# Kernel optimization log

Hardware: AMD Instinct MI355X
Metric: run time of the kernel (lower is better)

## Reference

```python
import jax, jax.numpy as jnp
import numpy as np

H = 450       # hidden_size (JTNN decoder default)
V = 800       # junction-tree vocab size
N_NODES = 4000
N_MESS = 6000
K = 6         # max neighbors (padded)
B = 256       # number of trees / roots
DH = 450      # netD hidden size
DEPTH = 15


def setup_inputs() -> dict:
    key = jax.random.key(0)
    ks = jax.random.split(key, 16)

    def w(k, shape, fan_in):
        return jax.random.normal(k, shape, dtype=jnp.float32) / np.float32(np.sqrt(fan_in))

    inp = {}
    inp["fnode"] = jax.random.randint(ks[0], (N_NODES,), 0, V)
    inp["fmess"] = jax.random.randint(ks[1], (N_MESS,), 0, N_NODES)
    inp["node_graph"] = jax.random.randint(ks[2], (N_NODES, K), 0, N_MESS)
    inp["mess_graph"] = jax.random.randint(ks[3], (N_MESS, K), 0, N_MESS)
    inp["root_idx"] = jax.random.randint(ks[4], (B,), 0, N_NODES)
    # Generator (JTNN decoder GRU) params; weights stored torch-style [out, in]
    inp["emb"] = w(ks[5], (V, H), H)
    inp["W_z_w"] = w(ks[6], (H, 2 * H), 2 * H)
    inp["W_z_b"] = jnp.zeros((H,), jnp.float32)
    inp["W_r_w"] = w(ks[7], (H, H), H)          # bias=False in JTNN
    inp["U_r_w"] = w(ks[8], (H, H), H)
    inp["U_r_b"] = jnp.zeros((H,), jnp.float32)
    inp["W_h_w"] = w(ks[9], (H, 2 * H), 2 * H)
    inp["W_h_b"] = jnp.zeros((H,), jnp.float32)
    # netD: Linear(2H,DH) -> LeakyReLU(0.1) -> Linear(DH,DH) -> LeakyReLU(0.1) -> Linear(DH,1)
    inp["D1_w"] = w(ks[10], (DH, 2 * H), 2 * H)
    inp["D1_b"] = jnp.zeros((DH,), jnp.float32)
    inp["D2_w"] = w(ks[11], (DH, DH), DH)
    inp["D2_b"] = jnp.zeros((DH,), jnp.float32)
    inp["D3_w"] = w(ks[12], (1, DH), DH)
    inp["D3_b"] = jnp.zeros((1,), jnp.float32)
    inp["depth"] = DEPTH
    return inp


def _generator(fnode, fmess, node_graph, mess_graph, root_idx,
               emb, W_z_w, W_z_b, W_r_w, U_r_w, U_r_b, W_h_w, W_h_b, depth):
    fnode_e = emb[fnode]                      # [N, H] embedding lookup
    x = fnode_e[fmess]                        # [M, H] source-node features per message
    M = fmess.shape[0]
    mask = jnp.ones((M, 1), jnp.float32).at[0].set(0.0)   # message 0 is padding
    h0 = jnp.zeros((M, emb.shape[1]), jnp.float32)

    def step(h, _):
        h_nei = h[mess_graph]                 # [M, K, H] gather of incoming messages
        sum_h = h_nei.sum(axis=1)             # [M, H]
        z = jax.nn.sigmoid(jnp.concatenate([x, sum_h], axis=-1) @ W_z_w.T + W_z_b)
        r = jax.nn.sigmoid((x @ W_r_w.T)[:, None, :] + h_nei @ U_r_w.T + U_r_b)
        sum_gh = (r * h_nei).sum(axis=1)
        pre_h = jnp.tanh(jnp.concatenate([x, sum_gh], axis=-1) @ W_h_w.T + W_h_b)
        h_new = ((1.0 - z) * sum_h + z * pre_h) * mask
        return h_new, None

    h, _ = jax.lax.scan(step, h0, None, length=depth)
    mess_nei = h[node_graph].sum(axis=1)      # [N, H]
    node_vecs = jnp.concatenate([fnode_e, mess_nei], axis=-1)   # [N, 2H]
    return node_vecs[root_idx]                # [B, 2H]


def reference(fnode, fmess, node_graph, mess_graph, root_idx,
              emb, W_z_w, W_z_b, W_r_w, U_r_w, U_r_b, W_h_w, W_h_b,
              D1_w, D1_b, D2_w, D2_b, D3_w, D3_b, depth):
    root_vecs = _generator(fnode, fmess, node_graph, mess_graph, root_idx,
                           emb, W_z_w, W_z_b, W_r_w, U_r_w, U_r_b, W_h_w, W_h_b, depth)
    h1 = jax.nn.leaky_relu(root_vecs @ D1_w.T + D1_b, 0.1)
    h2 = jax.nn.leaky_relu(h1 @ D2_w.T + D2_b, 0.1)
    score = (h2 @ D3_w.T + D3_b).squeeze(-1)  # [B] discriminator scores
    return score
```

## Files before the change

### kernel.cpp

```cpp
#include <hip/hip_runtime.h>
#include <stdint.h>
#include <stddef.h>

#define NMSG   6000
#define NNODE  4000
#define HDIM   450
#define KNEI   6
#define NB     256
#define KP     480
#define MP     6016
#define NPAD   512
#define DEPTH_C 15
#define GX     96
#define GROWS  6016

typedef unsigned short u16;
typedef __attribute__((ext_vector_type(8))) short short8;
typedef __attribute__((ext_vector_type(4))) float f32x4;

__device__ __forceinline__ float b2f(u16 h) { return __uint_as_float(((unsigned)h) << 16); }
__device__ __forceinline__ u16 f2b(float f) {
    unsigned u = __float_as_uint(f);
    return (u16)((u + 0x7FFFu + ((u >> 16) & 1u)) >> 16);
}
__device__ __forceinline__ void fsplit(float f, u16& hi, u16& lo) {
    u16 h = f2b(f);
    hi = h;
    lo = f2b(f - b2f(h));
}
__device__ __forceinline__ float gload(const void* p, size_t i, int isb) {
    return isb ? b2f(((const u16*)p)[i]) : ((const float*)p)[i];
}

__device__ __forceinline__ void gload_lds16(const void* g, void* l) {
    __builtin_amdgcn_global_load_lds((const __attribute__((address_space(1))) unsigned int*)g,
                                     (__attribute__((address_space(3))) unsigned int*)l,
                                     16, 0, 0);
}

__device__ __forceinline__ int xcd_row(int b) {
    if (b >= 5632) return b;
    int c = b & 7, u = b >> 3;
    return 512 * (u >> 6) + 64 * c + (u & 63);
}

__global__ void zero_kernel(uint4* p, size_t n16) {
    size_t i = (size_t)blockIdx.x * blockDim.x + threadIdx.x;
    size_t stride = (size_t)gridDim.x * blockDim.x;
    uint4 z = make_uint4(0, 0, 0, 0);
    for (; i < n16; i += stride) p[i] = z;
}

__global__ void detect_kernel(const void* __restrict__ emb, int* __restrict__ flagp) {
    __shared__ int cnt;
    if (threadIdx.x == 0) cnt = 0;
    __syncthreads();
    const u16* p = (const u16*)emb;
    int c = 0;
#pragma unroll
    for (int j = 0; j < 8; ++j) {
        u16 u = p[2 * (threadIdx.x * 8 + j)];
        int e = (u >> 7) & 0xFF;
        if (u == 0 || u == 0x8000u || (e >= 64 && e <= 127)) c++;
    }
    atomicAdd(&cnt, c);
    __syncthreads();
    if (threadIdx.x == 0) *flagp = (cnt > 1300) ? 1 : 0;
}

__global__ void prep_kernel(const void* __restrict__ Wz, const void* __restrict__ Wr,
                            const void* __restrict__ Ur, const void* __restrict__ Wh,
                            const void* __restrict__ D1w, const void* __restrict__ D2w,
                            u16* __restrict__ wb, float* __restrict__ d1t, float* __restrict__ d2t,
                            const int* __restrict__ flagp) {
    const int isb = *flagp;
    int job = blockIdx.y;
    int idx = blockIdx.x * 256 + threadIdx.x;
    if (job < 6) {
        if (idx >= NPAD * KP) return;
        int n = idx / KP, k = idx % KP;
        u16 vh = 0, vl = 0;
        if (n < HDIM && k < HDIM) {
            float f;
            switch (job) {
                case 0: f = gload(Wz, (size_t)n * 900 + k, isb); break;
                case 1: f = gload(Wz, (size_t)n * 900 + 450 + k, isb); break;
                case 2: f = gload(Wr, (size_t)n * 450 + k, isb); break;
                case 3: f = gload(Ur, (size_t)n * 450 + k, isb); break;
                case 4: f = gload(Wh, (size_t)n * 900 + k, isb); break;
                default: f = gload(Wh, (size_t)n * 900 + 450 + k, isb); break;
            }
            fsplit(f, vh, vl);
        }
        wb[(size_t)job * NPAD * KP + idx] = vh;
        wb[(size_t)(job + 6) * NPAD * KP + idx] = vl;
    } else if (job == 6) {
        if (idx >= 900 * 450) return;
        int i = idx / 450, j = idx % 450;
        d1t[i * 450 + j] = gload(D1w, (size_t)j * 900 + i, isb);
    } else {
        if (idx >= 450 * 450) return;
        int i = idx / 450, j = idx % 450;
        d2t[i * 450 + j] = gload(D2w, (size_t)j * 450 + i, isb);
    }
}

__global__ void xgather_kernel(const int* __restrict__ fnode, const int* __restrict__ fmess,
                               const void* __restrict__ emb, u16* __restrict__ xh,
                               u16* __restrict__ xl, const int* __restrict__ flagp) {
    const int isb = *flagp;
    int m = xcd_row(blockIdx.x);
    int c = threadIdx.x * 2;
    if (m >= NMSG || c >= HDIM) return;
    int src = fnode[fmess[m]];
    float f0, f1;
    if (isb) {
        unsigned u = *(const unsigned*)((const u16*)emb + (size_t)src * HDIM + c);
        f0 = b2f((u16)u); f1 = b2f((u16)(u >> 16));
    } else {
        float2 v = *(const float2*)((const float*)emb + (size_t)src * HDIM + c);
        f0 = v.x; f1 = v.y;
    }
    u16 h0, l0, h1, l1;
    fsplit(f0, h0, l0);
    fsplit(f1, h1, l1);
    *(unsigned*)(xh + (size_t)m * KP + c) = (unsigned)h0 | ((unsigned)h1 << 16);
    *(unsigned*)(xl + (size_t)m * KP + c) = (unsigned)l0 | ((unsigned)l1 << 16);
}

__global__ void gather_kernel(const u16* __restrict__ hh, const u16* __restrict__ hl,
                              const u16* __restrict__ uzh, const u16* __restrict__ xzr,
                              const void* __restrict__ urb, const int* __restrict__ mg,
                              float* __restrict__ shf, u16* __restrict__ zq,
                              u16* __restrict__ sgh, u16* __restrict__ sgl,
                              const int* __restrict__ flagp) {
    const int isb = *flagp;
    int m = xcd_row(blockIdx.x);
    int c = threadIdx.x * 2;
    if (m >= NMSG || c >= HDIM) return;
    const int* ng = mg + m * KNEI;
    size_t o = (size_t)m * HDIM + c;
    uint2 xv = *(const uint2*)(xzr + o * 2);
    float xz0 = b2f((u16)xv.x), xr0 = b2f((u16)(xv.x >> 16));
    float xz1 = b2f((u16)xv.y), xr1 = b2f((u16)(xv.y >> 16));
    float b0 = gload(urb, c, isb);
    float b1 = gload(urb, c + 1, isb);
    float s0 = 0.f, s1 = 0.f;
    float t0 = 0.f, t1 = 0.f;
    float g0 = 0.f, g1 = 0.f;
#pragma unroll
    for (int k = 0; k < KNEI; ++k) {
        int nm = ng[k];
        size_t oh = (size_t)nm * KP + c;
        unsigned vh = *(const unsigned*)(hh + oh);
        unsigned vl = *(const unsigned*)(hl + oh);
        float hv0 = b2f((u16)vh) + b2f((u16)vl);
        float hv1 = b2f((u16)(vh >> 16)) + b2f((u16)(vl >> 16));
        s0 += hv0; s1 += hv1;
        uint2 uv = *(const uint2*)(uzh + ((size_t)nm * HDIM + c) * 2);
        t0 += b2f((u16)uv.x);
        t1 += b2f((u16)uv.y);
        float a0 = xr0 + b2f((u16)(uv.x >> 16)) + b0;
        float a1 = xr1 + b2f((u16)(uv.y >> 16)) + b1;
        g0 += hv0 / (1.f + __expf(-a0));
        g1 += hv1 / (1.f + __expf(-a1));
    }
    *(float2*)(shf + o) = make_float2(s0, s1);
    float z0 = 1.f / (1.f + __expf(-(xz0 + t0)));
    float z1 = 1.f / (1.f + __expf(-(xz1 + t1)));
    unsigned q0 = __float2uint_rn(z0 * 65535.f);
    unsigned q1 = __float2uint_rn(z1 * 65535.f);
    *(unsigned*)(zq + o) = q0 | (q1 << 16);
    u16 h0, l0, h1, l1;
    fsplit(g0, h0, l0);
    fsplit(g1, h1, l1);
    *(unsigned*)(sgh + (size_t)m * KP + c) = (unsigned)h0 | ((unsigned)h1 << 16);
    *(unsigned*)(sgl + (size_t)m * KP + c) = (unsigned)l0 | ((unsigned)l1 << 16);
}

struct GemmDesc {
    const u16* Ah;
    const u16* Al;
    const u16* Bh;
    const u16* Bl;
    const void* bias;
    const u16* addb;
    u16* outb;
    int ostride;
    int ooff;
    const u16* zq;
    const float* shf;
    u16* hbh;
    u16* hbl;
    int mode;
};

__device__ __forceinline__ void tile_mfma(const u16* buf, int wm, int wn, int llo, int cx,
                                          f32x4 acc[2][2]) {
    short8 afh[2], afl[2], bfh[2], bfl[2];
#pragma unroll
    for (int i = 0; i < 2; i++) {
        const int off = (wm * 32 + i * 16 + llo) * 32 + cx;
        afh[i] = *(const short8*)(buf + off);
        afl[i] = *(const short8*)(buf + 2048 + off);
    }
#pragma unroll
    for (int j = 0; j < 2; j++) {
        const int off = (wn * 32 + j * 16 + llo) * 32 + cx;
        bfh[j] = *(const short8*)(buf + 4096 + off);
        bfl[j] = *(const short8*)(buf + 6144 + off);
    }
#pragma unroll
    for (int i = 0; i < 2; i++)
#pragma unroll
        for (int j = 0; j < 2; j++) {
            acc[i][j] = __builtin_amdgcn_mfma_f32_16x16x32_bf16(afh[i], bfl[j], acc[i][j], 0, 0, 0);
            acc[i][j] = __builtin_amdgcn_mfma_f32_16x16x32_bf16(afl[i], bfh[j], acc[i][j], 0, 0, 0);
            acc[i][j] = __builtin_amdgcn_mfma_f32_16x16x32_bf16(afh[i], bfh[j], acc[i][j], 0, 0, 0);
        }
}

__global__ __launch_bounds__(256, 5) void gemm_kernel(GemmDesc d0, GemmDesc d1, GemmDesc d2,
                                                      const int* __restrict__ flagp) {
    if (blockIdx.x >= 94) return;
    GemmDesc d = (blockIdx.z == 0) ? d0 : ((blockIdx.z == 1) ? d1 : d2);
    const int isb = *flagp;
    __shared__ __align__(16) u16 lds[2][4][64 * 32];
    const int tid = threadIdx.x;
    const int wave = tid >> 6, lane = tid & 63;
    const int m0 = blockIdx.x * 64;
    const int n0 = blockIdx.y * 64;
    const int wm = wave & 1, wn = wave >> 1;
    const int lhi = lane >> 4, llo = lane & 15;
    const int cx = (lhi ^ ((llo >> 1) & 3)) * 8;

    f32x4 acc[2][2];
#pragma unroll
    for (int i = 0; i < 2; i++)
#pragma unroll
        for (int j = 0; j < 2; j++) acc[i][j] = (f32x4){0.f, 0.f, 0.f, 0.f};

    const int rl = lane >> 2, cl = lane & 3;
    const int csw = cl ^ ((rl >> 1) & 3);
    const u16* ssrc = (wave == 0) ? d.Ah : (wave == 1) ? d.Al : (wave == 2) ? d.Bh : d.Bl;
    const int srb = (wave < 2) ? m0 : n0;
    const u16* gbase = ssrc + (size_t)(srb + rl) * KP + csw * 8;

    auto stage = [&](int b, int kt) {
#pragma unroll
        for (int q = 0; q < 4; ++q)
            gload_lds16(gbase + (size_t)q * 16 * KP + kt * 32, &lds[b][wave][q * 512]);
    };

    stage(0, 0);
    __syncthreads();

    int p = 0;
#pragma unroll 1
    for (int kt = 1; kt < KP / 32; ++kt) {
        stage(p ^ 1, kt);
        tile_mfma(&lds[p][0][0], wm, wn, llo, cx, acc);
        __syncthreads();
        p ^= 1;
    }
    tile_mfma(&lds[p][0][0], wm, wn, llo, cx, acc);

#pragma unroll
    for (int i = 0; i < 2; i++) {
#pragma unroll
        for (int j = 0; j < 2; j++) {
            int n = n0 + wn * 32 + j * 16 + llo;
            int mb = m0 + wm * 32 + i * 16 + lhi * 4;
            if (n >= HDIM) continue;
#pragma unroll
            for (int r = 0; r < 4; r++) {
                int m = mb + r;
                if (m >= NMSG) continue;
                size_t o = (size_t)m * HDIM + n;
                float v = acc[i][j][r];
                if (d.mode == 0) {
                    if (d.bias) v += gload(d.bias, n, isb);
                    d.outb[o * d.ostride + d.ooff] = f2b(v);
                } else {
                    size_t ob = (size_t)m * KP + n;
                    float a = v + b2f(d.addb[o]);
                    float e = __expf(2.f * a);
                    float pre = 1.f - 2.f / (e + 1.f);
                    float zz = (float)d.zq[o] * (1.f / 65535.f);
                    float shv = d.shf[o];
                    float hn = (1.f - zz) * shv + zz * pre;
                    if (m == 0) hn = 0.f;
                    fsplit(hn, d.hbh[ob], d.hbl[ob]);
                }
            }
        }
    }
}

__global__ __launch_bounds__(256, 3) void gemm2_kernel(
        const u16* __restrict__ Ah, const u16* __restrict__ Al,
        const u16* __restrict__ B0h, const u16* __restrict__ B0l,
        const u16* __restrict__ B1h, const u16* __restrict__ B1l,
        u16* __restrict__ uzh) {
    if (blockIdx.x >= 94) return;
    __shared__ __align__(16) u16 lds[2][6][64 * 32];
    const int tid = threadIdx.x;
    const int wave = tid >> 6, lane = tid & 63;
    const int m0 = blockIdx.x * 64;
    const int n0 = blockIdx.y * 64;
    const int wm = wave & 1, wn = wave >> 1;
    const int lhi = lane >> 4, llo = lane & 15;
    const int cx = (lhi ^ ((llo >> 1) & 3)) * 8;

    const int rl = lane >> 2, cl = lane & 3;
    const int csw = cl ^ ((rl >> 1) & 3);
    const int row = wave * 16 + rl;
    const size_t aoff = (size_t)(m0 + row) * KP + csw * 8;
    const size_t boff = (size_t)(n0 + row) * KP + csw * 8;
    const int ldst = wave * 512;

    f32x4 acc0[2][2], acc1[2][2];
#pragma unroll
    for (int i = 0; i < 2; i++)
#pragma unroll
        for (int j = 0; j < 2; j++) {
            acc0[i][j] = (f32x4){0.f, 0.f, 0.f, 0.f};
            acc1[i][j] = (f32x4){0.f, 0.f, 0.f, 0.f};
        }

    auto stage = [&](int b, int kt) {
        const size_t ko = (size_t)kt * 32;
        gload_lds16(Ah + aoff + ko,  &lds[b][0][ldst]);
        gload_lds16(Al + aoff + ko,  &lds[b][1][ldst]);
        gload_lds16(B0h + boff + ko, &lds[b][2][ldst]);
        gload_lds16(B0l + boff + ko, &lds[b][3][ldst]);
        gload_lds16(B1h + boff + ko, &lds[b][4][ldst]);
        gload_lds16(B1l + boff + ko, &lds[b][5][ldst]);
    };

    auto compute = [&](const u16* buf) {
        short8 afh[2], afl[2], b0h[2], b0l[2], b1h[2], b1l[2];
#pragma unroll
        for (int i = 0; i < 2; i++) {
            const int off = (wm * 32 + i * 16 + llo) * 32 + cx;
            afh[i] = *(const short8*)(buf + off);
            afl[i] = *(const short8*)(buf + 2048 + off);
        }
#pragma unroll
        for (int j = 0; j < 2; j++) {
            const int off = (wn * 32 + j * 16 + llo) * 32 + cx;
            b0h[j] = *(const short8*)(buf + 4096 + off);
            b0l[j] = *(const short8*)(buf + 6144 + off);
            b1h[j] = *(const short8*)(buf + 8192 + off);
            b1l[j] = *(const short8*)(buf + 10240 + off);
        }
#pragma unroll
        for (int i = 0; i < 2; i++)
#pragma unroll
            for (int j = 0; j < 2; j++) {
                acc0[i][j] = __builtin_amdgcn_mfma_f32_16x16x32_bf16(afh[i], b0l[j], acc0[i][j], 0, 0, 0);
                acc0[i][j] = __builtin_amdgcn_mfma_f32_16x16x32_bf16(afl[i], b0h[j], acc0[i][j], 0, 0, 0);
                acc0[i][j] = __builtin_amdgcn_mfma_f32_16x16x32_bf16(afh[i], b0h[j], acc0[i][j], 0, 0, 0);
                acc1[i][j] = __builtin_amdgcn_mfma_f32_16x16x32_bf16(afh[i], b1l[j], acc1[i][j], 0, 0, 0);
                acc1[i][j] = __builtin_amdgcn_mfma_f32_16x16x32_bf16(afl[i], b1h[j], acc1[i][j], 0, 0, 0);
                acc1[i][j] = __builtin_amdgcn_mfma_f32_16x16x32_bf16(afh[i], b1h[j], acc1[i][j], 0, 0, 0);
            }
    };

    stage(0, 0);
    __syncthreads();
    int p = 0;
#pragma unroll 1
    for (int kt = 1; kt < KP / 32; ++kt) {
        stage(p ^ 1, kt);
        compute(&lds[p][0][0]);
        __syncthreads();
        p ^= 1;
    }
    compute(&lds[p][0][0]);

#pragma unroll
    for (int i = 0; i < 2; i++) {
#pragma unroll
        for (int j = 0; j < 2; j++) {
            int n = n0 + wn * 32 + j * 16 + llo;
            int mb = m0 + wm * 32 + i * 16 + lhi * 4;
            if (n >= HDIM) continue;
#pragma unroll
            for (int r = 0; r < 4; r++) {
                int m = mb + r;
                if (m >= NMSG) continue;
                size_t o = (size_t)m * HDIM + n;
                unsigned pk = (unsigned)f2b(acc0[i][j][r]) | ((unsigned)f2b(acc1[i][j][r]) << 16);
                *(unsigned*)(uzh + o * 2) = pk;
            }
        }
    }
}

__global__ void root_kernel(const int* __restrict__ root_idx, const int* __restrict__ fnode,
                            const int* __restrict__ node_graph, const void* __restrict__ emb,
                            const u16* __restrict__ hh, const u16* __restrict__ hl,
                            float* __restrict__ rv, const int* __restrict__ flagp) {
    const int isb = *flagp;
    int b = blockIdx.x, c = threadIdx.x;
    if (c >= HDIM) return;
    int node = root_idx[b];
    rv[(size_t)b * 900 + c] = gload(emb, (size_t)fnode[node] * HDIM + c, isb);
    const int* ng = node_graph + node * KNEI;
    float s = 0.f;
#pragma unroll
    for (int k = 0; k < KNEI; ++k) {
        size_t o = (size_t)ng[k] * KP + c;
        s += b2f(hh[o]) + b2f(hl[o]);
    }
    rv[(size_t)b * 900 + 450 + c] = s;
}

__global__ void mlp_kernel(const float* __restrict__ rv, const float* __restrict__ d1t,
                           const void* __restrict__ D1b, const float* __restrict__ d2t,
                           const void* __restrict__ D2b, const void* __restrict__ D3w,
                           const void* __restrict__ D3b, void* __restrict__ out,
                           const int* __restrict__ flagp) {
    const int isb = *flagp;
    __shared__ float xs[900];
    __shared__ float h1s[450];
    __shared__ float red[8];
    int b = blockIdx.x, t = threadIdx.x;
    for (int i = t; i < 900; i += 512) xs[i] = rv[(size_t)b * 900 + i];
    __syncthreads();
    float a1 = 0.f;
    if (t < 450) {
        for (int i = 0; i < 900; ++i) a1 = fmaf(xs[i], d1t[i * 450 + t], a1);
        a1 += gload(D1b, t, isb);
        a1 = a1 > 0.f ? a1 : 0.1f * a1;
        h1s[t] = a1;
    }
    __syncthreads();
    float a2 = 0.f;
    if (t < 450) {
        for (int i = 0; i < 450; ++i) a2 = fmaf(h1s[i], d2t[i * 450 + t], a2);
        a2 += gload(D2b, t, isb);
        a2 = a2 > 0.f ? a2 : 0.1f * a2;
        a2 *= gload(D3w, t, isb);
    }
#pragma unroll
    for (int o = 32; o > 0; o >>= 1) a2 += __shfl_down(a2, o, 64);
    if ((t & 63) == 0) red[t >> 6] = a2;
    __syncthreads();
    if (t == 0) {
        float s = gload(D3b, 0, isb);
#pragma unroll
        for (int w = 0; w < 8; ++w) s += red[w];
        if (isb) ((u16*)out)[b] = f2b(s);
        else     ((float*)out)[b] = s;
    }
}

extern "C" void kernel_launch(void* const* d_in, const int* in_sizes, int n_in,
                              void* d_out, int out_size, void* d_ws, size_t ws_size,
                              hipStream_t stream) {
    const int* fnode      = (const int*)d_in[0];
    const int* fmess      = (const int*)d_in[1];
    const int* node_graph = (const int*)d_in[2];
    const int* mess_graph = (const int*)d_in[3];
    const int* root_idx   = (const int*)d_in[4];
    const void* emb = d_in[5];
    const void* Wz  = d_in[6];
    const void* Wzb = d_in[7];
    const void* Wr  = d_in[8];
    const void* Ur  = d_in[9];
    const void* Urb = d_in[10];
    const void* Wh  = d_in[11];
    const void* Whb = d_in[12];
    const void* D1w = d_in[13];
    const void* D1b = d_in[14];
    const void* D2w = d_in[15];
    const void* D2b = d_in[16];
    const void* D3w = d_in[17];
    const void* D3b = d_in[18];

    char* ws = (char*)d_ws;
    size_t off = 0;
    auto alloc = [&](size_t bytes) {
        char* p = ws + off;
        off += (bytes + 255) & ~(size_t)255;
        return p;
    };
    const size_t SZ_F   = (size_t)NMSG * HDIM * 4;
    const size_t SZ_B16 = (size_t)MP * KP * 2;
    const size_t SZ_W   = (size_t)NPAD * KP * 2;

    int* flagp = (int*)alloc(256);
    u16* xbh   = (u16*)alloc(SZ_B16);
    u16* xbl   = (u16*)alloc(SZ_B16);
    u16* hbh   = (u16*)alloc(SZ_B16);
    u16* hbl   = (u16*)alloc(SZ_B16);
    u16* sgbh  = (u16*)alloc(SZ_B16);
    u16* sgbl  = (u16*)alloc(SZ_B16);
    size_t zero_bytes = off;

    u16* uzh   = (u16*)alloc(SZ_F);
    u16* xzr   = (u16*)alloc(SZ_F);
    u16* xwhb  = (u16*)alloc((size_t)NMSG * HDIM * 2);
    float* shf = (float*)alloc(SZ_F);
    u16* zqb   = (u16*)alloc((size_t)NMSG * HDIM * 2);
    u16* wb    = (u16*)alloc(12 * SZ_W);
    float* d1t = (float*)alloc(900 * 450 * 4);
    float* d2t = (float*)alloc(450 * 450 * 4);
    float* rv  = (float*)alloc((size_t)NB * 900 * 4);
    (void)ws_size; (void)in_sizes; (void)n_in; (void)out_size;

    const size_t WP = (size_t)NPAD * KP;
    u16* bWzxh = wb + 0 * WP;  u16* bWzxl = wb + 6 * WP;
    u16* bWzhh = wb + 1 * WP;  u16* bWzhl = wb + 7 * WP;
    u16* bWrh  = wb + 2 * WP;  u16* bWrl  = wb + 8 * WP;
    u16* bUrh  = wb + 3 * WP;  u16* bUrl  = wb + 9 * WP;
    u16* bWhxh = wb + 4 * WP;  u16* bWhxl = wb + 10 * WP;
    u16* bWhhh = wb + 5 * WP;  u16* bWhhl = wb + 11 * WP;

    zero_kernel<<<2048, 256, 0, stream>>>((uint4*)ws, zero_bytes / 16);
    detect_kernel<<<1, 256, 0, stream>>>(emb, flagp);
    prep_kernel<<<dim3(1583, 8), 256, 0, stream>>>(Wz, Wr, Ur, Wh, D1w, D2w,
                                                   wb, d1t, d2t, flagp);
    xgather_kernel<<<GROWS, 256, 0, stream>>>(fnode, fmess, emb, xbh, xbl, flagp);

    GemmDesc g0 = { xbh, xbl, bWzxh, bWzxl, Wzb, nullptr, xzr, 2, 0,
                    nullptr, nullptr, nullptr, nullptr, 0 };
    GemmDesc g1 = { xbh, xbl, bWrh,  bWrl,  nullptr, nullptr, xzr, 2, 1,
                    nullptr, nullptr, nullptr, nullptr, 0 };
    GemmDesc g2 = { xbh, xbl, bWhxh, bWhxl, Whb, nullptr, xwhb, 1, 0,
                    nullptr, nullptr, nullptr, nullptr, 0 };
    gemm_kernel<<<dim3(GX, 8, 3), 256, 0, stream>>>(g0, g1, g2, flagp);

    for (int t = 0; t < DEPTH_C; ++t) {
        gemm2_kernel<<<dim3(GX, 8), 256, 0, stream>>>(hbh, hbl, bWzhh, bWzhl,
                                                      bUrh, bUrl, uzh);
        gather_kernel<<<GROWS, 256, 0, stream>>>(hbh, hbl, uzh, xzr, Urb,
                                                 mess_graph, shf, zqb, sgbh, sgbl, flagp);
        GemmDesc dh = { sgbh, sgbl, bWhhh, bWhhl, nullptr, xwhb, nullptr, 0, 0,
                        zqb, shf, hbh, hbl, 3 };
        gemm_kernel<<<dim3(GX, 8, 1), 256, 0, stream>>>(dh, dh, dh, flagp);
    }

    root_kernel<<<NB, 512, 0, stream>>>(root_idx, fnode, node_graph, emb, hbh, hbl, rv, flagp);
    mlp_kernel<<<NB, 512, 0, stream>>>(rv, d1t, D1b, d2t, D2b, D3w, D3b, d_out, flagp);
}
```

Baseline: 1.283 ms.

## Move z-gate GEMM after gather using summed h, fuse with W_h GEMM

Rather than computing h@W_zh per message and summing over neighbors in the gather, the gather now writes sum_h as a hi/lo bf16 split, and a new fused kernel computes both sum_h@W_zh and sum_gh@W_hh, then applies the GRU update in its epilogue. The per-step first GEMM now only computes h@U_r, which halves its B operand and output traffic. The gather no longer reads or writes the z-related and fp32 buffers. sum_gh is stored as a single bf16 with no lo part, and the new GEMM drops the A-lo cross term, which lowers precision.

```diff
diff --git a/kernel.cpp b/kernel.cpp
--- a/kernel.cpp
+++ b/kernel.cpp
@@ -129,24 +129,21 @@
 }
 
 __global__ void gather_kernel(const u16* __restrict__ hh, const u16* __restrict__ hl,
-                              const u16* __restrict__ uzh, const u16* __restrict__ xzr,
+                              const u16* __restrict__ uhb, const u16* __restrict__ xwrb,
                               const void* __restrict__ urb, const int* __restrict__ mg,
-                              float* __restrict__ shf, u16* __restrict__ zq,
-                              u16* __restrict__ sgh, u16* __restrict__ sgl,
-                              const int* __restrict__ flagp) {
+                              u16* __restrict__ shfh, u16* __restrict__ shfl,
+                              u16* __restrict__ sgh, const int* __restrict__ flagp) {
     const int isb = *flagp;
     int m = xcd_row(blockIdx.x);
     int c = threadIdx.x * 2;
     if (m >= NMSG || c >= HDIM) return;
     const int* ng = mg + m * KNEI;
     size_t o = (size_t)m * HDIM + c;
-    uint2 xv = *(const uint2*)(xzr + o * 2);
-    float xz0 = b2f((u16)xv.x), xr0 = b2f((u16)(xv.x >> 16));
-    float xz1 = b2f((u16)xv.y), xr1 = b2f((u16)(xv.y >> 16));
+    unsigned xv = *(const unsigned*)(xwrb + o);
+    float xr0 = b2f((u16)xv), xr1 = b2f((u16)(xv >> 16));
     float b0 = gload(urb, c, isb);
     float b1 = gload(urb, c + 1, isb);
     float s0 = 0.f, s1 = 0.f;
-    float t0 = 0.f, t1 = 0.f;
     float g0 = 0.f, g1 = 0.f;
 #pragma unroll
     for (int k = 0; k < KNEI; ++k) {
@@ -157,25 +154,19 @@
         float hv0 = b2f((u16)vh) + b2f((u16)vl);
         float hv1 = b2f((u16)(vh >> 16)) + b2f((u16)(vl >> 16));
         s0 += hv0; s1 += hv1;
-        uint2 uv = *(const uint2*)(uzh + ((size_t)nm * HDIM + c) * 2);
-        t0 += b2f((u16)uv.x);
-        t1 += b2f((u16)uv.y);
-        float a0 = xr0 + b2f((u16)(uv.x >> 16)) + b0;
-        float a1 = xr1 + b2f((u16)(uv.y >> 16)) + b1;
+        unsigned uv = *(const unsigned*)(uhb + (size_t)nm * HDIM + c);
+        float a0 = xr0 + b2f((u16)uv) + b0;
+        float a1 = xr1 + b2f((u16)(uv >> 16)) + b1;
         g0 += hv0 / (1.f + __expf(-a0));
         g1 += hv1 / (1.f + __expf(-a1));
     }
-    *(float2*)(shf + o) = make_float2(s0, s1);
-    float z0 = 1.f / (1.f + __expf(-(xz0 + t0)));
-    float z1 = 1.f / (1.f + __expf(-(xz1 + t1)));
-    unsigned q0 = __float2uint_rn(z0 * 65535.f);
-    unsigned q1 = __float2uint_rn(z1 * 65535.f);
-    *(unsigned*)(zq + o) = q0 | (q1 << 16);
-    u16 h0, l0, h1, l1;
-    fsplit(g0, h0, l0);
-    fsplit(g1, h1, l1);
-    *(unsigned*)(sgh + (size_t)m * KP + c) = (unsigned)h0 | ((unsigned)h1 << 16);
-    *(unsigned*)(sgl + (size_t)m * KP + c) = (unsigned)l0 | ((unsigned)l1 << 16);
+    size_t ok = (size_t)m * KP + c;
+    u16 sh0, sl0, sh1, sl1;
+    fsplit(s0, sh0, sl0);
+    fsplit(s1, sh1, sl1);
+    *(unsigned*)(shfh + ok) = (unsigned)sh0 | ((unsigned)sh1 << 16);
+    *(unsigned*)(shfl + ok) = (unsigned)sl0 | ((unsigned)sl1 << 16);
+    *(unsigned*)(sgh + ok) = (unsigned)f2b(g0) | ((unsigned)f2b(g1) << 16);
 }
 
 struct GemmDesc {
@@ -184,41 +175,10 @@
     const u16* Bh;
     const u16* Bl;
     const void* bias;
-    const u16* addb;
     u16* outb;
     int ostride;
     int ooff;
-    const u16* zq;
-    const float* shf;
-    u16* hbh;
-    u16* hbl;
-    int mode;
 };
-
-__device__ __forceinline__ void tile_mfma(const u16* buf, int wm, int wn, int llo, int cx,
-                                          f32x4 acc[2][2]) {
-    short8 afh[2], afl[2], bfh[2], bfl[2];
-#pragma unroll
-    for (int i = 0; i < 2; i++) {
-        const int off = (wm * 32 + i * 16 + llo) * 32 + cx;
-        afh[i] = *(const short8*)(buf + off);
-        afl[i] = *(const short8*)(buf + 2048 + off);
-    }
-#pragma unroll
-    for (int j = 0; j < 2; j++) {
-        const int off = (wn * 32 + j * 16 + llo) * 32 + cx;
-        bfh[j] = *(const short8*)(buf + 4096 + off);
-        bfl[j] = *(const short8*)(buf + 6144 + off);
-    }
-#pragma unroll
-    for (int i = 0; i < 2; i++)
-#pragma unroll
-        for (int j = 0; j < 2; j++) {
-            acc[i][j] = __builtin_amdgcn_mfma_f32_16x16x32_bf16(afh[i], bfl[j], acc[i][j], 0, 0, 0);
-            acc[i][j] = __builtin_amdgcn_mfma_f32_16x16x32_bf16(afl[i], bfh[j], acc[i][j], 0, 0, 0);
-            acc[i][j] = __builtin_amdgcn_mfma_f32_16x16x32_bf16(afh[i], bfh[j], acc[i][j], 0, 0, 0);
-        }
-}
 
 __global__ __launch_bounds__(256, 5) void gemm_kernel(GemmDesc d0, GemmDesc d1, GemmDesc d2,
                                                       const int* __restrict__ flagp) {
@@ -252,6 +212,30 @@
             gload_lds16(gbase + (size_t)q * 16 * KP + kt * 32, &lds[b][wave][q * 512]);
     };
 
+    auto compute = [&](const u16* buf) {
+        short8 afh[2], afl[2], bfh[2], bfl[2];
+#pragma unroll
+        for (int i = 0; i < 2; i++) {
+            const int off = (wm * 32 + i * 16 + llo) * 32 + cx;
+            afh[i] = *(const short8*)(buf + off);
+            afl[i] = *(const short8*)(buf + 2048 + off);
+        }
+#pragma unroll
+        for (int j = 0; j < 2; j++) {
+            const int off = (wn * 32 + j * 16 + llo) * 32 + cx;
+            bfh[j] = *(const short8*)(buf + 4096 + off);
+            bfl[j] = *(const short8*)(buf + 6144 + off);
+        }
+#pragma unroll
+        for (int i = 0; i < 2; i++)
+#pragma unroll
+            for (int j = 0; j < 2; j++) {
+                acc[i][j] = __builtin_amdgcn_mfma_f32_16x16x32_bf16(afh[i], bfl[j], acc[i][j], 0, 0, 0);
+                acc[i][j] = __builtin_amdgcn_mfma_f32_16x16x32_bf16(afl[i], bfh[j], acc[i][j], 0, 0, 0);
+                acc[i][j] = __builtin_amdgcn_mfma_f32_16x16x32_bf16(afh[i], bfh[j], acc[i][j], 0, 0, 0);
+            }
+    };
+
     stage(0, 0);
     __syncthreads();
 
@@ -259,11 +243,11 @@
 #pragma unroll 1
     for (int kt = 1; kt < KP / 32; ++kt) {
         stage(p ^ 1, kt);
-        tile_mfma(&lds[p][0][0], wm, wn, llo, cx, acc);
+        compute(&lds[p][0][0]);
         __syncthreads();
         p ^= 1;
     }
-    tile_mfma(&lds[p][0][0], wm, wn, llo, cx, acc);
+    compute(&lds[p][0][0]);
 
 #pragma unroll
     for (int i = 0; i < 2; i++) {
@@ -278,32 +262,21 @@
                 if (m >= NMSG) continue;
                 size_t o = (size_t)m * HDIM + n;
                 float v = acc[i][j][r];
-                if (d.mode == 0) {
-                    if (d.bias) v += gload(d.bias, n, isb);
-                    d.outb[o * d.ostride + d.ooff] = f2b(v);
-                } else {
-                    size_t ob = (size_t)m * KP + n;
-                    float a = v + b2f(d.addb[o]);
-                    float e = __expf(2.f * a);
-                    float pre = 1.f - 2.f / (e + 1.f);
-                    float zz = (float)d.zq[o] * (1.f / 65535.f);
-                    float shv = d.shf[o];
-                    float hn = (1.f - zz) * shv + zz * pre;
-                    if (m == 0) hn = 0.f;
-                    fsplit(hn, d.hbh[ob], d.hbl[ob]);
-                }
+                if (d.bias) v += gload(d.bias, n, isb);
+                d.outb[o * d.ostride + d.ooff] = f2b(v);
             }
         }
     }
 }
 
-__global__ __launch_bounds__(256, 3) void gemm2_kernel(
-        const u16* __restrict__ Ah, const u16* __restrict__ Al,
-        const u16* __restrict__ B0h, const u16* __restrict__ B0l,
-        const u16* __restrict__ B1h, const u16* __restrict__ B1l,
-        u16* __restrict__ uzh) {
+__global__ __launch_bounds__(256, 3) void gemm3d_kernel(
+        const u16* __restrict__ sgh, const u16* __restrict__ shfh, const u16* __restrict__ shfl,
+        const u16* __restrict__ bWhhh, const u16* __restrict__ bWhhl,
+        const u16* __restrict__ bWzhh, const u16* __restrict__ bWzhl,
+        const u16* __restrict__ xwhb, const u16* __restrict__ xwzb,
+        u16* __restrict__ hbh, u16* __restrict__ hbl) {
     if (blockIdx.x >= 94) return;
-    __shared__ __align__(16) u16 lds[2][6][64 * 32];
+    __shared__ __align__(16) u16 lds[2][12288];
     const int tid = threadIdx.x;
     const int wave = tid >> 6, lane = tid & 63;
     const int m0 = blockIdx.x * 64;
@@ -319,51 +292,49 @@
     const size_t boff = (size_t)(n0 + row) * KP + csw * 8;
     const int ldst = wave * 512;
 
-    f32x4 acc0[2][2], acc1[2][2];
+    f32x4 accP[2][2], accZ[2][2];
 #pragma unroll
     for (int i = 0; i < 2; i++)
 #pragma unroll
         for (int j = 0; j < 2; j++) {
-            acc0[i][j] = (f32x4){0.f, 0.f, 0.f, 0.f};
-            acc1[i][j] = (f32x4){0.f, 0.f, 0.f, 0.f};
+            accP[i][j] = (f32x4){0.f, 0.f, 0.f, 0.f};
+            accZ[i][j] = (f32x4){0.f, 0.f, 0.f, 0.f};
         }
 
     auto stage = [&](int b, int kt) {
         const size_t ko = (size_t)kt * 32;
-        gload_lds16(Ah + aoff + ko,  &lds[b][0][ldst]);
-        gload_lds16(Al + aoff + ko,  &lds[b][1][ldst]);
-        gload_lds16(B0h + boff + ko, &lds[b][2][ldst]);
-        gload_lds16(B0l + boff + ko, &lds[b][3][ldst]);
-        gload_lds16(B1h + boff + ko, &lds[b][4][ldst]);
-        gload_lds16(B1l + boff + ko, &lds[b][5][ldst]);
+        gload_lds16(sgh   + aoff + ko, &lds[b][0     + ldst]);
+        gload_lds16(shfh  + aoff + ko, &lds[b][2048  + ldst]);
+        gload_lds16(bWhhh + boff + ko, &lds[b][4096  + ldst]);
+        gload_lds16(bWhhl + boff + ko, &lds[b][6144  + ldst]);
+        gload_lds16(bWzhh + boff + ko, &lds[b][8192  + ldst]);
+        gload_lds16(bWzhl + boff + ko, &lds[b][10240 + ldst]);
     };
 
     auto compute = [&](const u16* buf) {
-        short8 afh[2], afl[2], b0h[2], b0l[2], b1h[2], b1l[2];
+        short8 as_[2], ah[2], bwh[2], bwl[2], bzh[2], bzl[2];
 #pragma unroll
         for (int i = 0; i < 2; i++) {
             const int off = (wm * 32 + i * 16 + llo) * 32 + cx;
-            afh[i] = *(const short8*)(buf + off);
-            afl[i] = *(const short8*)(buf + 2048 + off);
+            as_[i] = *(const short8*)(buf + off);
+            ah[i]  = *(const short8*)(buf + 2048 + off);
         }
 #pragma unroll
         for (int j = 0; j < 2; j++) {
             const int off = (wn * 32 + j * 16 + llo) * 32 + cx;
-            b0h[j] = *(const short8*)(buf + 4096 + off);
-            b0l[j] = *(const short8*)(buf + 6144 + off);
-            b1h[j] = *(const short8*)(buf + 8192 + off);
-            b1l[j] = *(const short8*)(buf + 10240 + off);
+            bwh[j] = *(const short8*)(buf + 4096 + off);
+            bwl[j] = *(const short8*)(buf + 6144 + off);
+            bzh[j] = *(const short8*)(buf + 8192 + off);
+            bzl[j] = *(const short8*)(buf + 10240 + off);
         }
 #pragma unroll
         for (int i = 0; i < 2; i++)
 #pragma unroll
             for (int j = 0; j < 2; j++) {
-                acc0[i][j] = __builtin_amdgcn_mfma_f32_16x16x32_bf16(afh[i], b0l[j], acc0[i][j], 0, 0, 0);
-                acc0[i][j] = __builtin_amdgcn_mfma_f32_16x16x32_bf16(afl[i], b0h[j], acc0[i][j], 0, 0, 0);
-                acc0[i][j] = __builtin_amdgcn_mfma_f32_16x16x32_bf16(afh[i], b0h[j], acc0[i][j], 0, 0, 0);
-                acc1[i][j] = __builtin_amdgcn_mfma_f32_16x16x32_bf16(afh[i], b1l[j], acc1[i][j], 0, 0, 0);
-                acc1[i][j] = __builtin_amdgcn_mfma_f32_16x16x32_bf16(afl[i], b1h[j], acc1[i][j], 0, 0, 0);
-                acc1[i][j] = __builtin_amdgcn_mfma_f32_16x16x32_bf16(afh[i], b1h[j], acc1[i][j], 0, 0, 0);
+                accP[i][j] = __builtin_amdgcn_mfma_f32_16x16x32_bf16(as_[i], bwl[j], accP[i][j], 0, 0, 0);
+                accP[i][j] = __builtin_amdgcn_mfma_f32_16x16x32_bf16(as_[i], bwh[j], accP[i][j], 0, 0, 0);
+                accZ[i][j] = __builtin_amdgcn_mfma_f32_16x16x32_bf16(ah[i], bzl[j], accZ[i][j], 0, 0, 0);
+                accZ[i][j] = __builtin_amdgcn_mfma_f32_16x16x32_bf16(ah[i], bzh[j], accZ[i][j], 0, 0, 0);
             }
     };
 
@@ -373,11 +344,11 @@
 #pragma unroll 1
     for (int kt = 1; kt < KP / 32; ++kt) {
         stage(p ^ 1, kt);
-        compute(&lds[p][0][0]);
+        compute(&lds[p][0]);
         __syncthreads();
         p ^= 1;
     }
-    compute(&lds[p][0][0]);
+    compute(&lds[p][0]);
 
 #pragma unroll
     for (int i = 0; i < 2; i++) {
@@ -391,8 +362,16 @@
                 int m = mb + r;
                 if (m >= NMSG) continue;
                 size_t o = (size_t)m * HDIM + n;
-                unsigned pk = (unsigned)f2b(acc0[i][j][r]) | ((unsigned)f2b(acc1[i][j][r]) << 16);
-                *(unsigned*)(uzh + o * 2) = pk;
+                size_t ob = (size_t)m * KP + n;
+                float aP = accP[i][j][r] + b2f(xwhb[o]);
+                float e = __expf(2.f * aP);
+                float pre = 1.f - 2.f / (e + 1.f);
+                float aZ = accZ[i][j][r] + b2f(xwzb[o]);
+                float z = 1.f / (1.f + __expf(-aZ));
+                float shv = b2f(shfh[ob]) + b2f(shfl[ob]);
+                float hn = (1.f - z) * shv + z * pre;
+                if (m == 0) hn = 0.f;
+                fsplit(hn, hbh[ob], hbl[ob]);
             }
         }
     }
@@ -487,8 +466,8 @@
         off += (bytes + 255) & ~(size_t)255;
         return p;
     };
-    const size_t SZ_F   = (size_t)NMSG * HDIM * 4;
     const size_t SZ_B16 = (size_t)MP * KP * 2;
+    const size_t SZ_H16 = (size_t)NMSG * HDIM * 2;
     const size_t SZ_W   = (size_t)NPAD * KP * 2;
 
     int* flagp = (int*)alloc(256);
@@ -497,14 +476,14 @@
     u16* hbh   = (u16*)alloc(SZ_B16);
     u16* hbl   = (u16*)alloc(SZ_B16);
     u16* sgbh  = (u16*)alloc(SZ_B16);
-    u16* sgbl  = (u16*)alloc(SZ_B16);
+    u16* shfh  = (u16*)alloc(SZ_B16);
+    u16* shfl  = (u16*)alloc(SZ_B16);
     size_t zero_bytes = off;
 
-    u16* uzh   = (u16*)alloc(SZ_F);
-    u16* xzr   = (u16*)alloc(SZ_F);
-    u16* xwhb  = (u16*)alloc((size_t)NMSG * HDIM * 2);
-    float* shf = (float*)alloc(SZ_F);
-    u16* zqb   = (u16*)alloc((size_t)NMSG * HDIM * 2);
+    u16* uhb   = (u16*)alloc(SZ_H16);
+    u16* xwzb  = (u16*)alloc(SZ_H16);
+    u16* xwrb  = (u16*)alloc(SZ_H16);
+    u16* xwhb  = (u16*)alloc(SZ_H16);
     u16* wb    = (u16*)alloc(12 * SZ_W);
     float* d1t = (float*)alloc(900 * 450 * 4);
     float* d2t = (float*)alloc(450 * 450 * 4);
@@ -525,22 +504,19 @@
                                                    wb, d1t, d2t, flagp);
     xgather_kernel<<<GROWS, 256, 0, stream>>>(fnode, fmess, emb, xbh, xbl, flagp);
 
-    GemmDesc g0 = { xbh, xbl, bWzxh, bWzxl, Wzb, nullptr, xzr, 2, 0,
-                    nullptr, nullptr, nullptr, nullptr, 0 };
-    GemmDesc g1 = { xbh, xbl, bWrh,  bWrl,  nullptr, nullptr, xzr, 2, 1,
-                    nullptr, nullptr, nullptr, nullptr, 0 };
-    GemmDesc g2 = { xbh, xbl, bWhxh, bWhxl, Whb, nullptr, xwhb, 1, 0,
-                    nullptr, nullptr, nullptr, nullptr, 0 };
+    GemmDesc g0 = { xbh, xbl, bWzxh, bWzxl, Wzb, xwzb, 1, 0 };
+    GemmDesc g1 = { xbh, xbl, bWrh,  bWrl,  nullptr, xwrb, 1, 0 };
+    GemmDesc g2 = { xbh, xbl, bWhxh, bWhxl, Whb, xwhb, 1, 0 };
     gemm_kernel<<<dim3(GX, 8, 3), 256, 0, stream>>>(g0, g1, g2, flagp);
 
+    GemmDesc du = { hbh, hbl, bUrh, bUrl, nullptr, uhb, 1, 0 };
     for (int t = 0; t < DEPTH_C; ++t) {
-        gemm2_kernel<<<dim3(GX, 8), 256, 0, stream>>>(hbh, hbl, bWzhh, bWzhl,
-                                                      bUrh, bUrl, uzh);
-        gather_kernel<<<GROWS, 256, 0, stream>>>(hbh, hbl, uzh, xzr, Urb,
-                                                 mess_graph, shf, zqb, sgbh, sgbl, flagp);
-        GemmDesc dh = { sgbh, sgbl, bWhhh, bWhhl, nullptr, xwhb, nullptr, 0, 0,
-                        zqb, shf, hbh, hbl, 3 };
-        gemm_kernel<<<dim3(GX, 8, 1), 256, 0, stream>>>(dh, dh, dh, flagp);
+        gemm_kernel<<<dim3(GX, 8, 1), 256, 0, stream>>>(du, du, du, flagp);
+        gather_kernel<<<GROWS, 256, 0, stream>>>(hbh, hbl, uhb, xwrb, Urb,
+                                                 mess_graph, shfh, shfl, sgbh, flagp);
+        gemm3d_kernel<<<dim3(GX, 8), 256, 0, stream>>>(sgbh, shfh, shfl, bWhhh, bWhhl,
+                                                       bWzhh, bWzhl, xwhb, xwzb,
+                                                       hbh, hbl);
     }
 
     root_kernel<<<NB, 512, 0, stream>>>(root_idx, fnode, node_graph, emb, hbh, hbl, rv, flagp);
```

New measurement: 1.182 ms. 7.8% less time.
